# Performance work log

Measured on AMD Instinct MI355X. Metric: run time of the kernel, lower is better.

Reference implementation:

```python
import jax, jax.numpy as jnp
import numpy as np

N = 17
H = 8
DIRECT = np.array([[0,1],[1,2],[2,3],[0,4],[4,5],[5,6],[0,7],[7,8],[8,9],[9,10],[8,11],[11,12],[12,13],[8,14],[14,15],[15,16]])
SYM = np.array([[1,4],[2,5],[3,6],[11,14],[12,15],[13,16]])


def _base_mask(dw, sw, cw):
    # static skeleton bias: ones + direct-connect + symmetric + self-connect weights
    m = jnp.ones((N, N), jnp.float32)
    m = m.at[DIRECT[:, 0], DIRECT[:, 1]].add(dw)
    m = m.at[SYM[:, 0], SYM[:, 1]].add(sw)
    m = m.at[SYM[:, 1], SYM[:, 0]].add(sw)
    return m + cw * jnp.eye(N, dtype=jnp.float32)


def _ln_custom(x, g, b, eps=1e-6):
    # custom LayerNorm: unbiased std (torch .std default), eps added to std
    mu = x.mean(-1, keepdims=True)
    var = ((x - mu) ** 2).sum(-1, keepdims=True) / (x.shape[-1] - 1)
    return g * (x - mu) / (jnp.sqrt(var) + eps) + b


def _ln_std(x, g, b, eps=1e-5):
    # standard nn.LayerNorm (biased var, eps inside sqrt)
    mu = x.mean(-1, keepdims=True)
    var = ((x - mu) ** 2).mean(-1, keepdims=True)
    return g * (x - mu) * jax.lax.rsqrt(var + eps) + b


def _forward(mask, x, pre_3d, c, wq, bq, wk, bk, wv, bv, wo, bo, sa_w1, sa_b1, sa_g1, sa_sb1, sa_w2, sa_b2, sa_g2, sa_sb2, jrp_w, jrp_b, direct_w, sym_w, self_w, dyn_scale, A_hat, g1_w, g1_b, g2_w, g2_b, n1_g, n1_b, n2_g, n2_b, ada1_w, ada1_b, ada2_w, ada2_b):
    B, _, D = x.shape
    dk = D // H
    inv = 1.0 / np.sqrt(dk)
    mflag = (mask == 0)[:, None]                       # [B,1,N,N]
    sil_c = jax.nn.silu(c)
    for i in range(wq.shape[0]):                       # small fixed layer count
        # --- sublayer 0: adaLN-modulated skeleton-biased self-attention ---
        sh1, sc1, gt1 = jnp.split(sil_c @ ada1_w[i] + ada1_b[i], 3, axis=2)
        xin = _ln_custom(x, n1_g[i], n1_b[i]) * (1 + sc1) + sh1
        Q = (pre_3d @ wq[i] + bq[i]).reshape(B, N, H, dk).transpose(0, 2, 1, 3)
        K = (xin @ wk[i] + bk[i]).reshape(B, N, H, dk).transpose(0, 2, 1, 3)
        V = (xin @ wv[i] + bv[i]).reshape(B, N, H, dk).transpose(0, 2, 1, 3)
        scores = jnp.einsum('bhqd,bhkd->bhqk', Q, K) * inv
        # dynamic skeleton mask from query features (pre_3d)
        jf = jax.nn.relu(_ln_std(pre_3d @ sa_w1[i] + sa_b1[i], sa_g1[i], sa_sb1[i]))
        jf = jax.nn.relu(_ln_std(jf @ sa_w2[i] + sa_b2[i], sa_g2[i], sa_sb2[i]))
        dyn = jax.nn.sigmoid(jf @ jrp_w[i] + jrp_b[i]) * dyn_scale[i]   # [B,N,N]
        skel = _base_mask(direct_w[i], sym_w[i], self_w[i])[None] + dyn
        guided = jnp.where(mflag, -1e9, scores * skel[:, None])
        p = jax.nn.softmax(guided, axis=-1)
        att = jnp.einsum('bhqk,bhkd->bhqd', p, V).transpose(0, 2, 1, 3).reshape(B, N, D)
        x = x + gt1 * (att @ wo[i] + bo[i])
        # --- sublayer 1: adaLN-modulated GraphNet (2 Laplacian gconvs) ---
        sh2, sc2, gt2 = jnp.split(sil_c @ ada2_w[i] + ada2_b[i], 3, axis=2)
        y = _ln_custom(x, n2_g[i], n2_b[i]) * (1 + sc2) + sh2
        a = A_hat[i]
        dh = (a.sum(0) + 1e-5) ** -0.5                  # column-degree^{-1/2}
        Lm = dh[:, None] * a * dh[None, :]
        y0 = jax.nn.relu(jnp.einsum('ij,bjd->bid', Lm, y) @ g1_w[i] + g1_b[i])
        y1 = jnp.einsum('ij,bjd->bid', Lm, y0) @ g2_w[i] + g2_b[i]
        x = x + gt2 * y1
    return x


def setup_inputs():
    B, D, Lyr = 4096, 256, 2
    ki = iter(jax.random.split(jax.random.key(0), 32))
    rn = lambda *s: jax.random.normal(next(ki), s, jnp.float32) * 0.02
    z = lambda *s: jnp.zeros(s, jnp.float32)
    o = lambda *s: jnp.ones(s, jnp.float32)
    return {
        'x': jax.random.normal(next(ki), (B, N, D), jnp.float32),
        'pre_3d': jax.random.normal(next(ki), (B, N, D), jnp.float32),
        'c': jax.random.normal(next(ki), (B, N, D), jnp.float32),
        'mask': jnp.ones((B, N, N), jnp.int32),
        'wq': rn(Lyr, D, D), 'bq': z(Lyr, D),
        'wk': rn(Lyr, D, D), 'bk': z(Lyr, D),
        'wv': rn(Lyr, D, D), 'bv': z(Lyr, D),
        'wo': rn(Lyr, D, D), 'bo': z(Lyr, D),
        'sa_w1': rn(Lyr, D, D // 2), 'sa_b1': z(Lyr, D // 2),
        'sa_g1': o(Lyr, D // 2), 'sa_sb1': z(Lyr, D // 2),
        'sa_w2': rn(Lyr, D // 2, D // 4), 'sa_b2': z(Lyr, D // 4),
        'sa_g2': o(Lyr, D // 4), 'sa_sb2': z(Lyr, D // 4),
        'jrp_w': rn(Lyr, D // 4, N), 'jrp_b': z(Lyr, N),
        'direct_w': jnp.full((Lyr,), 2.0, jnp.float32),
        'sym_w': jnp.full((Lyr,), 1.5, jnp.float32),
        'self_w': jnp.full((Lyr,), 3.0, jnp.float32),
        'dyn_scale': jnp.full((Lyr,), 0.5, jnp.float32),
        'A_hat': jnp.tile(jnp.eye(N, dtype=jnp.float32)[None], (Lyr, 1, 1)),
        'g1_w': rn(Lyr, D, 2 * D), 'g1_b': z(Lyr, 2 * D),
        'g2_w': rn(Lyr, 2 * D, D), 'g2_b': z(Lyr, D),
        'n1_g': o(Lyr, D), 'n1_b': z(Lyr, D),
        'n2_g': o(Lyr, D), 'n2_b': z(Lyr, D),
        'ada1_w': rn(Lyr, D, 3 * D), 'ada1_b': z(Lyr, 3 * D),
        'ada2_w': rn(Lyr, D, 3 * D), 'ada2_b': z(Lyr, 3 * D),
    }


def reference(x, pre_3d, c, mask, wq, bq, wk, bk, wv, bv, wo, bo, sa_w1, sa_b1, sa_g1, sa_sb1, sa_w2, sa_b2, sa_g2, sa_sb2, jrp_w, jrp_b, direct_w, sym_w, self_w, dyn_scale, A_hat, g1_w, g1_b, g2_w, g2_b, n1_g, n1_b, n2_g, n2_b, ada1_w, ada1_b, ada2_w, ada2_b):
    return _forward(mask, x, pre_3d, c, wq, bq, wk, bk, wv, bv, wo, bo, sa_w1, sa_b1, sa_g1, sa_sb1, sa_w2, sa_b2, sa_g2, sa_sb2, jrp_w, jrp_b, direct_w, sym_w, self_w, dyn_scale, A_hat, g1_w, g1_b, g2_w, g2_b, n1_g, n1_b, n2_g, n2_b, ada1_w, ada1_b, ada2_w, ada2_b)
```

## Files before the change

### kernel.cpp

```cpp
#include <hip/hip_runtime.h>
#include <stdint.h>


#define BATCH 4096
#define NJ 17
#define NHEAD 8

typedef __bf16 bf16x8 __attribute__((ext_vector_type(8)));
typedef float f32x4 __attribute__((ext_vector_type(4)));

__device__ __forceinline__ float bf2f(unsigned short u){
  union { unsigned int i; float f; } v; v.i = ((unsigned int)u) << 16; return v.f;
}
__device__ __forceinline__ unsigned short f2bf(float f){
  union { float f; unsigned int i; } v; v.f = f;
  unsigned int i = v.i;
  return (unsigned short)((i + 0x7fffu + ((i >> 16) & 1u)) >> 16);
}
__device__ __forceinline__ float blo(unsigned int v){ union{unsigned int i;float f;}x; x.i=v<<16; return x.f; }
__device__ __forceinline__ float bhi(unsigned int v){ union{unsigned int i;float f;}x; x.i=v&0xffff0000u; return x.f; }

__device__ __forceinline__ void gload_lds16(const void* g, void* l) {
  __builtin_amdgcn_global_load_lds(
      (const __attribute__((address_space(1))) unsigned int*)g,
      (__attribute__((address_space(3))) unsigned int*)l, 16, 0, 0);
}

__global__ __launch_bounds__(256) void prep_kernel(
    const float* __restrict__ pre, const float* __restrict__ c,
    unsigned short* __restrict__ pre_bf, unsigned short* __restrict__ silc_bf)
{
  size_t i = (size_t)(blockIdx.x*256 + threadIdx.x)*4;
  float4 p = *(const float4*)(pre + i);
  float4 cv = *(const float4*)(c + i);
  float s0 = cv.x/(1.f+__expf(-cv.x));
  float s1 = cv.y/(1.f+__expf(-cv.y));
  float s2 = cv.z/(1.f+__expf(-cv.z));
  float s3 = cv.w/(1.f+__expf(-cv.w));
  uint2 po, so;
  po.x = (unsigned)f2bf(p.x) | ((unsigned)f2bf(p.y)<<16);
  po.y = (unsigned)f2bf(p.z) | ((unsigned)f2bf(p.w)<<16);
  so.x = (unsigned)f2bf(s0) | ((unsigned)f2bf(s1)<<16);
  so.y = (unsigned)f2bf(s2) | ((unsigned)f2bf(s3)<<16);
  *(uint2*)(pre_bf + i) = po;
  *(uint2*)(silc_bf + i) = so;
}

struct TJob { const float* src; unsigned short* dst; int K; int N; };
struct TJobs { TJob j[22]; };

__global__ __launch_bounds__(256) void transpose_kernel(TJobs jobs)
{
  TJob jb = jobs.j[blockIdx.y];
  int total = jb.K * jb.N;
  int idx = blockIdx.x*256 + threadIdx.x;
  if (idx >= total) return;
  int n = idx / jb.K;
  int k = idx - n*jb.K;
  jb.dst[idx] = f2bf(jb.src[(size_t)k*jb.N + n]);
}

__global__ void lm_kernel(const float* __restrict__ A_hat, float* __restrict__ LmOut)
{
  int L = blockIdx.x;
  const float* a = A_hat + L*289;
  float* Lm = LmOut + L*289;
  __shared__ float dh[17];
  int t = threadIdx.x;
  if (t < 17) {
    float s = 0;
    for (int i = 0; i < 17; i++) s += a[i*17 + t];
    dh[t] = 1.0f/sqrtf(s + 1e-5f);
  }
  __syncthreads();
  for (int i = t; i < 289; i += 64) {
    int qq = i/17, jj = i - qq*17;
    Lm[i] = dh[qq]*a[i]*dh[jj];
  }
}

__global__ __launch_bounds__(256) void lnmod_kernel(
    const float* __restrict__ x, const unsigned short* __restrict__ shsc,
    const float* __restrict__ g, const float* __restrict__ b,
    unsigned short* __restrict__ out)
{
  int row = blockIdx.x*4 + (threadIdx.x>>6);
  int lane = threadIdx.x & 63;
  const float4 v = *(const float4*)(x + (size_t)row*256 + lane*4);
  float s = v.x+v.y+v.z+v.w;
#pragma unroll
  for (int o=32;o;o>>=1) s += __shfl_down(s,o,64);
  float mu = __shfl(s,0,64) * (1.f/256.f);
  float d0=v.x-mu,d1=v.y-mu,d2=v.z-mu,d3=v.w-mu;
  float qq = d0*d0+d1*d1+d2*d2+d3*d3;
#pragma unroll
  for (int o=32;o;o>>=1) qq += __shfl_down(qq,o,64);
  qq = __shfl(qq,0,64);
  float rstd = 1.f/(sqrtf(qq*(1.f/255.f)) + 1e-6f);
  int c = lane*4;
  const float4 gv = *(const float4*)(g + c);
  const float4 bv = *(const float4*)(b + c);
  const uint2 shp = *(const uint2*)(shsc + (size_t)row*512 + c);
  const uint2 scp = *(const uint2*)(shsc + (size_t)row*512 + 256 + c);
  float o0 = (gv.x*d0*rstd + bv.x)*(1.f+blo(scp.x)) + blo(shp.x);
  float o1 = (gv.y*d1*rstd + bv.y)*(1.f+bhi(scp.x)) + bhi(shp.x);
  float o2 = (gv.z*d2*rstd + bv.z)*(1.f+blo(scp.y)) + blo(shp.y);
  float o3 = (gv.w*d3*rstd + bv.w)*(1.f+bhi(scp.y)) + bhi(shp.y);
  uint2 ov;
  ov.x = (unsigned)f2bf(o0) | ((unsigned)f2bf(o1)<<16);
  ov.y = (unsigned)f2bf(o2) | ((unsigned)f2bf(o3)<<16);
  *(uint2*)(out + (size_t)row*256 + c) = ov;
}

template<int C>
__global__ __launch_bounds__(256) void lnstd_relu_kernel(
    unsigned short* __restrict__ io, const float* __restrict__ g, const float* __restrict__ b)
{
  constexpr int EPL = C/64;
  int row = blockIdx.x*4 + (threadIdx.x>>6);
  int lane = threadIdx.x & 63;
  unsigned short* rp = io + (size_t)row*C + lane*EPL;
  float v[EPL];
  if constexpr (EPL == 2) { unsigned int u = *(const unsigned int*)rp; v[0]=blo(u); v[1]=bhi(u); }
  else { v[0] = bf2f(rp[0]); }
  float s = 0;
#pragma unroll
  for (int e=0;e<EPL;e++) s += v[e];
#pragma unroll
  for (int o=32;o;o>>=1) s += __shfl_down(s,o,64);
  float mu = __shfl(s,0,64) * (1.f/C);
  float qq = 0;
#pragma unroll
  for (int e=0;e<EPL;e++){ float d=v[e]-mu; qq += d*d; }
#pragma unroll
  for (int o=32;o;o>>=1) qq += __shfl_down(qq,o,64);
  qq = __shfl(qq,0,64);
  float rstd = rsqrtf(qq*(1.f/C) + 1e-5f);
  unsigned short ov[EPL];
#pragma unroll
  for (int e=0;e<EPL;e++){
    int ccol = lane*EPL + e;
    float o = fmaxf(g[ccol]*(v[e]-mu)*rstd + b[ccol], 0.f);
    ov[e] = f2bf(o);
  }
  if constexpr (EPL==2){ *(unsigned int*)rp = (unsigned)ov[0] | ((unsigned)ov[1]<<16); }
  else rp[0] = ov[0];
}

__global__ __launch_bounds__(256) void skel_kernel(
    const unsigned short* __restrict__ jf2, const unsigned short* __restrict__ jrpt,
    const float* __restrict__ jrp_b,
    const float* __restrict__ dwp, const float* __restrict__ swp,
    const float* __restrict__ cwp, const float* __restrict__ dsp,
    float* __restrict__ skel)
{
  int gid = blockIdx.x*256 + threadIdx.x;
  int row = gid / 17;
  int k = gid - row*17;
  int q = row % 17;
  const uint4* a = (const uint4*)(jf2 + (size_t)row*64);
  const uint4* w = (const uint4*)(jrpt + k*64);
  float acc = jrp_b[k];
#pragma unroll
  for (int c = 0; c < 8; c++) {
    uint4 ua = a[c], uw = w[c];
    acc += blo(ua.x)*blo(uw.x) + bhi(ua.x)*bhi(uw.x)
         + blo(ua.y)*blo(uw.y) + bhi(ua.y)*bhi(uw.y)
         + blo(ua.z)*blo(uw.z) + bhi(ua.z)*bhi(uw.z)
         + blo(ua.w)*blo(uw.w) + bhi(ua.w)*bhi(uw.w);
  }
  float sig = 1.f/(1.f + __expf(-acc));
  float base = 1.f;
  const int dqa[16] = {0,1,2,0,4,5,0,7,8,9,8,11,12,8,14,15};
  const int dka[16] = {1,2,3,4,5,6,7,8,9,10,11,12,13,14,15,16};
#pragma unroll
  for (int t = 0; t < 16; t++) if (q==dqa[t] && k==dka[t]) base += dwp[0];
  const int s0a[6] = {1,2,3,11,12,13};
  const int s1a[6] = {4,5,6,14,15,16};
#pragma unroll
  for (int t = 0; t < 6; t++) if ((q==s0a[t]&&k==s1a[t])||(q==s1a[t]&&k==s0a[t])) base += swp[0];
  if (q==k) base += cwp[0];
  skel[gid] = base + sig*dsp[0];
}

__device__ __forceinline__ void load16f(const unsigned short* p, float* f){
  const uint4* p4 = (const uint4*)p;
#pragma unroll
  for (int c=0;c<2;c++){
    uint4 u=p4[c];
    f[c*8+0]=blo(u.x); f[c*8+1]=bhi(u.x); f[c*8+2]=blo(u.y); f[c*8+3]=bhi(u.y);
    f[c*8+4]=blo(u.z); f[c*8+5]=bhi(u.z); f[c*8+6]=blo(u.w); f[c*8+7]=bhi(u.w);
  }
}

__global__ __launch_bounds__(320) void attn_kernel(
    const unsigned short* Q, const unsigned short* __restrict__ KV,
    const float* __restrict__ skel,
    const int* __restrict__ mask, unsigned short* att)
{
  __shared__ unsigned short kvs[17*512];
  __shared__ float sks[289];
  __shared__ int   mks[289];
  const int b = blockIdx.x;
  const int tid = threadIdx.x;

  const uint4* src = (const uint4*)(KV + (size_t)b*17*512);
  for (int i = tid; i < 1088; i += 320) ((uint4*)kvs)[i] = src[i];
  const float* skb = skel + (size_t)b*289;
  const int* mkb = mask + (size_t)b*289;
  for (int i = tid; i < 289; i += 320) { sks[i] = skb[i]; mks[i] = mkb[i]; }
  __syncthreads();
  if (tid >= 272) return;

  const int t2 = tid >> 1;
  const int dh = tid & 1;
  const int h = t2 / 17;
  const int q = t2 - h*17;
  const int col = h*32 + dh*16;
  size_t rq = ((size_t)(b*17+q))*256 + col;
  float qv[16];
  load16f(Q + rq, qv);

  float p[17];
  float mx = -3e38f;
#pragma unroll
  for (int k = 0; k < 17; k++) {
    const uint4* kp = (const uint4*)(kvs + k*512 + col);
    float s = 0;
#pragma unroll
    for (int c = 0; c < 2; c++) {
      uint4 u = kp[c];
      s += qv[c*8+0]*blo(u.x) + qv[c*8+1]*bhi(u.x)
         + qv[c*8+2]*blo(u.y) + qv[c*8+3]*bhi(u.y)
         + qv[c*8+4]*blo(u.z) + qv[c*8+5]*bhi(u.z)
         + qv[c*8+6]*blo(u.w) + qv[c*8+7]*bhi(u.w);
    }
    s += __shfl_xor(s, 1, 64);
    s *= 0.17677669529663687f;
    float gvl = (mks[q*17+k]==0) ? -1e9f : s*sks[q*17+k];
    p[k] = gvl;
    mx = fmaxf(mx, gvl);
  }
  float sum = 0;
#pragma unroll
  for (int k = 0; k < 17; k++){ p[k] = __expf(p[k]-mx); sum += p[k]; }
  float inv = 1.f/sum;
  float acc[16];
#pragma unroll
  for (int d=0; d<16; d++) acc[d]=0;
#pragma unroll
  for (int k = 0; k < 17; k++) {
    float pk = p[k]*inv;
    const uint4* vp = (const uint4*)(kvs + k*512 + 256 + col);
#pragma unroll
    for (int c=0;c<2;c++){
      uint4 u=vp[c];
      acc[c*8+0] += pk*blo(u.x); acc[c*8+1] += pk*bhi(u.x);
      acc[c*8+2] += pk*blo(u.y); acc[c*8+3] += pk*bhi(u.y);
      acc[c*8+4] += pk*blo(u.z); acc[c*8+5] += pk*bhi(u.z);
      acc[c*8+6] += pk*blo(u.w); acc[c*8+7] += pk*bhi(u.w);
    }
  }
  uint4 o[2];
#pragma unroll
  for (int c=0;c<2;c++){
    o[c].x = (unsigned)f2bf(acc[c*8+0]) | ((unsigned)f2bf(acc[c*8+1])<<16);
    o[c].y = (unsigned)f2bf(acc[c*8+2]) | ((unsigned)f2bf(acc[c*8+3])<<16);
    o[c].z = (unsigned)f2bf(acc[c*8+4]) | ((unsigned)f2bf(acc[c*8+5])<<16);
    o[c].w = (unsigned)f2bf(acc[c*8+6]) | ((unsigned)f2bf(acc[c*8+7])<<16);
  }
  uint4* op = (uint4*)(att + rq);
  op[0] = o[0]; op[1] = o[1];
}

template<int D>
__global__ __launch_bounds__(256) void lmapply_kernel(
    unsigned short* __restrict__ io, const float* __restrict__ Lm)
{
  __shared__ unsigned short ys[17*D];
  __shared__ float lms[289];
  int b = blockIdx.x;
  int tid = threadIdx.x;
  unsigned short* base = io + (size_t)b*17*D;
  constexpr int CH = 17*D/8;
  for (int i = tid; i < CH; i += 256) ((uint4*)ys)[i] = ((const uint4*)base)[i];
  for (int i = tid; i < 289; i += 256) lms[i] = Lm[i];
  __syncthreads();
#pragma unroll
  for (int c0 = 0; c0 < D; c0 += 256) {
    int c = c0 + tid;
    float yv[17];
#pragma unroll
    for (int j = 0; j < 17; j++) yv[j] = bf2f(ys[j*D + c]);
#pragma unroll
    for (int qi = 0; qi < 17; qi++) {
      float a = 0;
#pragma unroll
      for (int j = 0; j < 17; j++) a += lms[qi*17+j]*yv[j];
      base[qi*D + c] = f2bf(a);
    }
  }
}

template<int TM, int TN, int EPI>
__global__ __launch_bounds__(256) void gemm_kernel(
    const unsigned short* __restrict__ A, const unsigned short* __restrict__ Bt,
    const float* __restrict__ bias, unsigned short* __restrict__ outbf,
    float* __restrict__ x_io, const unsigned short* __restrict__ gt,
    int N, int K)
{
  int lane = threadIdx.x & 63;
  int wave = threadIdx.x >> 6;
  int lm = lane & 15, quad = lane >> 4;
  int wm0 = blockIdx.x*(2*TM*16) + (wave>>1)*(TM*16);
  int wn0 = blockIdx.y*(2*TN*16) + (wave&1)*(TN*16);
  const unsigned short* pa[TM];
  const unsigned short* pb[TN];
#pragma unroll
  for (int t=0;t<TM;t++) pa[t] = A + (size_t)(wm0 + t*16 + lm)*K + quad*8;
#pragma unroll
  for (int t=0;t<TN;t++) pb[t] = Bt + (size_t)(wn0 + t*16 + lm)*K + quad*8;
  f32x4 acc[TM][TN] = {};
  for (int kc = 0; kc < K; kc += 32) {
    bf16x8 af[TM], bfv[TN];
#pragma unroll
    for (int t=0;t<TM;t++) af[t] = *(const bf16x8*)(pa[t] + kc);
#pragma unroll
    for (int t=0;t<TN;t++) bfv[t] = *(const bf16x8*)(pb[t] + kc);
#pragma unroll
    for (int i=0;i<TM;i++)
#pragma unroll
      for (int j=0;j<TN;j++)
        acc[i][j] = __builtin_amdgcn_mfma_f32_16x16x32_bf16(af[i], bfv[j], acc[i][j], 0, 0, 0);
  }
#pragma unroll
  for (int j=0;j<TN;j++) {
    int col = wn0 + j*16 + lm;
    float bv = bias[col];
#pragma unroll
    for (int i=0;i<TM;i++) {
      int r0 = wm0 + i*16 + quad*4;
#pragma unroll
      for (int e=0;e<4;e++) {
        int rr = r0 + e;
        float v = acc[i][j][e] + bv;
        if (EPI == 0) {
          outbf[(size_t)rr*N + col] = f2bf(v);
        } else if (EPI == 1) {
          outbf[(size_t)rr*N + col] = f2bf(fmaxf(v, 0.f));
        } else {
          size_t xi = (size_t)rr*N + col;
          x_io[xi] += bf2f(gt[(size_t)rr*256 + col]) * v;
        }
      }
    }
  }
}

template<int EPI>
__global__ __launch_bounds__(256) void gemm_lds_kernel(
    const unsigned short* __restrict__ A, const unsigned short* __restrict__ Bt,
    const float* __restrict__ bias, const float* __restrict__ bias2,
    unsigned short* __restrict__ out1, int ld1,
    unsigned short* __restrict__ out2, int ld2, int splitN,
    float* __restrict__ x_io, const unsigned short* __restrict__ gt,
    int K)
{
  __shared__ unsigned short As[3][128*32];
  __shared__ unsigned short Bs[3][128*32];
  const int tid = threadIdx.x;
  const int lane = tid & 63;
  const int wave = tid >> 6;
  const int lm = lane & 15, quad = lane >> 4;

  const int gx = gridDim.x;
  const int nwg = gx * (int)gridDim.y;
  int flat = (int)blockIdx.y * gx + (int)blockIdx.x;
  int xcd = flat & 7, idx = flat >> 3;
  int qd = nwg >> 3, rm = nwg & 7;
  int wg = (xcd < rm ? xcd*(qd+1) : rm*(qd+1) + (xcd-rm)*qd) + idx;
  int by = wg / gx, bx = wg - by*gx;
  const int m0 = by * 128;
  const int n0 = bx * 128;
  const int wm = (wave >> 1) * 64;
  const int wn = (wave & 1) * 64;

  const int srow = tid >> 2;
  const int sslot = tid & 3;

  auto stage = [&](int buf, int kc) {
#pragma unroll
    for (int l = 0; l < 2; l++) {
      int rr = l*64 + srow;
      int gs = sslot ^ (rr & 3);
      gload_lds16(A + (size_t)(m0 + rr)*K + kc + gs*8, &As[buf][l*2048 + tid*8]);
      gload_lds16(Bt + (size_t)(n0 + rr)*K + kc + gs*8, &Bs[buf][l*2048 + tid*8]);
    }
  };

  const int nt = K >> 5;
  stage(0, 0);
  stage(1, 32);

  f32x4 acc[4][4] = {};
  for (int t = 0; t < nt; t++) {
    if (t + 2 < nt) {
      stage((t+2)%3, (t+2)*32);
      asm volatile("s_waitcnt vmcnt(8)" ::: "memory");
    } else if (t + 1 < nt) {
      asm volatile("s_waitcnt vmcnt(4)" ::: "memory");
    } else {
      asm volatile("s_waitcnt vmcnt(0)" ::: "memory");
    }
    __builtin_amdgcn_s_barrier();

    const unsigned short* as_ = As[t % 3];
    const unsigned short* bs_ = Bs[t % 3];
    bf16x8 af[4], bfv[4];
#pragma unroll
    for (int tt = 0; tt < 4; tt++) {
      int ra = wm + tt*16 + lm;
      af[tt]  = *(const bf16x8*)(as_ + ra*32 + ((quad ^ (ra & 3)) << 3));
      int rb = wn + tt*16 + lm;
      bfv[tt] = *(const bf16x8*)(bs_ + rb*32 + ((quad ^ (rb & 3)) << 3));
    }
#pragma unroll
    for (int i = 0; i < 4; i++)
#pragma unroll
      for (int j = 0; j < 4; j++)
        acc[i][j] = __builtin_amdgcn_mfma_f32_16x16x32_bf16(af[i], bfv[j], acc[i][j], 0, 0, 0);
    __builtin_amdgcn_s_barrier();
  }

#pragma unroll
  for (int j = 0; j < 4; j++) {
    int col = n0 + wn + j*16 + lm;
    float bv = (bias2 && col >= splitN) ? bias2[col - splitN] : bias[col];
#pragma unroll
    for (int i = 0; i < 4; i++) {
      int r0 = m0 + wm + i*16 + quad*4;
#pragma unroll
      for (int e = 0; e < 4; e++) {
        int rr = r0 + e;
        float v = acc[i][j][e] + bv;
        if (EPI == 0) {
          if (out2 && col >= splitN) out2[(size_t)rr*ld2 + (col - splitN)] = f2bf(v);
          else                       out1[(size_t)rr*ld1 + col] = f2bf(v);
        } else if (EPI == 1) {
          out1[(size_t)rr*ld1 + col] = f2bf(fmaxf(v, 0.f));
        } else {
          size_t xi = (size_t)rr*256 + col;
          x_io[xi] += bf2f(gt[xi]) * v;
        }
      }
    }
  }
}

extern "C" void kernel_launch(void* const* d_in, const int* in_sizes, int n_in,
                              void* d_out, int out_size, void* d_ws, size_t ws_size,
                              hipStream_t stream)
{
  const float* x_in = (const float*)d_in[0];
  const float* pre  = (const float*)d_in[1];
  const float* cc   = (const float*)d_in[2];
  const int*   mask = (const int*)d_in[3];
  const float* wq = (const float*)d_in[4];   const float* bq = (const float*)d_in[5];
  const float* wk = (const float*)d_in[6];   const float* bk = (const float*)d_in[7];
  const float* wv = (const float*)d_in[8];   const float* bvz = (const float*)d_in[9];
  const float* wo = (const float*)d_in[10];  const float* bo = (const float*)d_in[11];
  const float* sa_w1 = (const float*)d_in[12]; const float* sa_b1 = (const float*)d_in[13];
  const float* sa_g1 = (const float*)d_in[14]; const float* sa_sb1 = (const float*)d_in[15];
  const float* sa_w2 = (const float*)d_in[16]; const float* sa_b2 = (const float*)d_in[17];
  const float* sa_g2 = (const float*)d_in[18]; const float* sa_sb2 = (const float*)d_in[19];
  const float* jrp_w = (const float*)d_in[20]; const float* jrp_b = (const float*)d_in[21];
  const float* dwp = (const float*)d_in[22]; const float* swp = (const float*)d_in[23];
  const float* cwp = (const float*)d_in[24]; const float* dsp = (const float*)d_in[25];
  const float* A_hat = (const float*)d_in[26];
  const float* g1w = (const float*)d_in[27]; const float* g1b = (const float*)d_in[28];
  const float* g2w = (const float*)d_in[29]; const float* g2b = (const float*)d_in[30];
  const float* n1g = (const float*)d_in[31]; const float* n1b = (const float*)d_in[32];
  const float* n2g = (const float*)d_in[33]; const float* n2b = (const float*)d_in[34];
  const float* ada1w = (const float*)d_in[35]; const float* ada1b = (const float*)d_in[36];
  const float* ada2w = (const float*)d_in[37]; const float* ada2b = (const float*)d_in[38];

  char* ws = (char*)d_ws;
  size_t off = 0;
  auto alloc = [&](size_t bytes)->char* {
    char* p = ws + off; off = (off + bytes + 255) & ~(size_t)255; return p;
  };

  TJobs jobs;
  int ji = 0;
  auto addjob = [&](const float* src, unsigned short* dst, int Kd, int Nd) {
    jobs.j[ji].src = src; jobs.j[ji].dst = dst; jobs.j[ji].K = Kd; jobs.j[ji].N = Nd;
    ji++;
  };
  unsigned short *t_ada1[2], *t_qsa[2], *t_kv[2], *t_wo[2],
                 *t_sa2[2], *t_jrp[2], *t_g1[2], *t_g2[2], *t_ada2[2];
  for (int L = 0; L < 2; L++) {
    t_ada1[L] = (unsigned short*)alloc((size_t)768*256*2);
    addjob(ada1w + (size_t)L*256*768, t_ada1[L], 256, 768);
    t_qsa[L] = (unsigned short*)alloc((size_t)384*256*2);
    addjob(wq + (size_t)L*65536, t_qsa[L], 256, 256);
    addjob(sa_w1 + (size_t)L*256*128, t_qsa[L] + 256*256, 256, 128);
    t_kv[L] = (unsigned short*)alloc((size_t)512*256*2);
    addjob(wk + (size_t)L*65536, t_kv[L], 256, 256);
    addjob(wv + (size_t)L*65536, t_kv[L] + 256*256, 256, 256);
    t_wo[L] = (unsigned short*)alloc((size_t)256*256*2);
    addjob(wo + (size_t)L*65536, t_wo[L], 256, 256);
    t_sa2[L] = (unsigned short*)alloc((size_t)64*128*2);
    addjob(sa_w2 + (size_t)L*128*64, t_sa2[L], 128, 64);
    t_jrp[L] = (unsigned short*)alloc((size_t)17*64*2);
    addjob(jrp_w + (size_t)L*64*17, t_jrp[L], 64, 17);
    t_g1[L] = (unsigned short*)alloc((size_t)512*256*2);
    addjob(g1w + (size_t)L*256*512, t_g1[L], 256, 512);
    t_g2[L] = (unsigned short*)alloc((size_t)256*512*2);
    addjob(g2w + (size_t)L*512*256, t_g2[L], 512, 256);
    t_ada2[L] = (unsigned short*)alloc((size_t)768*256*2);
    addjob(ada2w + (size_t)L*256*768, t_ada2[L], 256, 768);
  }
  float* lmbuf = (float*)alloc(2*289*4);
  size_t fixed_bytes = off;

  int chunkB = BATCH;
  for (; chunkB > 256; chunkB >>= 1) {
    size_t R = (size_t)chunkB * NJ;
    if (fixed_bytes + R*3652 + 8*256 <= ws_size) break;
  }
  const size_t R = (size_t)chunkB * NJ;
  const int nchunks = BATCH / chunkB;

  unsigned short* pre_bf  = (unsigned short*)alloc(R*256*2);
  unsigned short* silc_bf = (unsigned short*)alloc(R*256*2);
  unsigned short* xinb    = (unsigned short*)alloc(R*256*2);
  unsigned short* qbuf    = (unsigned short*)alloc(R*256*2);
  unsigned short* gtbuf   = (unsigned short*)alloc(R*256*2);
  unsigned short* kvb     = (unsigned short*)alloc(R*512*2);
  float*          skelb   = (float*)alloc(R*NJ*4);

  unsigned short* jf1 = xinb;
  unsigned short* jf2 = xinb + R*128;

  float* xout = (float*)d_out;
  hipMemcpyAsync(xout, x_in, (size_t)BATCH*NJ*256*4, hipMemcpyDeviceToDevice, stream);
  transpose_kernel<<<dim3(768, 22), 256, 0, stream>>>(jobs);
  lm_kernel<<<2, 64, 0, stream>>>(A_hat, lmbuf);

  const int gX = (int)(R/128);
  const int g4 = (int)(R/4);

  for (int ch = 0; ch < nchunks; ch++) {
    const size_t r0 = (size_t)ch * R;
    const float* pre_c = pre + r0*256;
    const float* cc_c  = cc + r0*256;
    const int* mask_c  = mask + (size_t)ch*chunkB*289;
    float* x_c = xout + r0*256;

    prep_kernel<<<g4, 256, 0, stream>>>(pre_c, cc_c, pre_bf, silc_bf);

    for (int L = 0; L < 2; L++) {
      gemm_lds_kernel<0><<<dim3(6,gX),256,0,stream>>>(silc_bf, t_ada1[L],
          ada1b + L*768, nullptr, kvb, 512, gtbuf, 256, 512, nullptr, nullptr, 256);
      lnmod_kernel<<<g4,256,0,stream>>>(x_c, kvb, n1g + L*256, n1b + L*256, xinb);
      gemm_lds_kernel<0><<<dim3(4,gX),256,0,stream>>>(xinb, t_kv[L],
          bk + L*256, bvz + L*256, kvb, 512, nullptr, 0, 256, nullptr, nullptr, 256);
      gemm_lds_kernel<0><<<dim3(3,gX),256,0,stream>>>(pre_bf, t_qsa[L],
          bq + L*256, sa_b1 + L*128, qbuf, 256, jf1, 128, 256, nullptr, nullptr, 256);
      lnstd_relu_kernel<128><<<g4,256,0,stream>>>(jf1, sa_g1 + L*128, sa_sb1 + L*128);
      gemm_kernel<4,2,0><<<dim3(gX,1),256,0,stream>>>(jf1, t_sa2[L], sa_b2 + L*64, jf2, nullptr, nullptr, 64, 128);
      lnstd_relu_kernel<64><<<g4,256,0,stream>>>(jf2, sa_g2 + L*64, sa_sb2 + L*64);
      skel_kernel<<<(int)(R*NJ/256),256,0,stream>>>(jf2, t_jrp[L], jrp_b + L*17, dwp+L, swp+L, cwp+L, dsp+L, skelb);
      attn_kernel<<<chunkB,320,0,stream>>>(qbuf, kvb, skelb, mask_c, qbuf);
      gemm_lds_kernel<3><<<dim3(2,gX),256,0,stream>>>(qbuf, t_wo[L],
          bo + L*256, nullptr, nullptr, 0, nullptr, 0, 0, x_c, gtbuf, 256);
      gemm_lds_kernel<0><<<dim3(6,gX),256,0,stream>>>(silc_bf, t_ada2[L],
          ada2b + L*768, nullptr, kvb, 512, gtbuf, 256, 512, nullptr, nullptr, 256);
      lnmod_kernel<<<g4,256,0,stream>>>(x_c, kvb, n2g + L*256, n2b + L*256, xinb);
      lmapply_kernel<256><<<chunkB,256,0,stream>>>(xinb, lmbuf + L*289);
      gemm_lds_kernel<1><<<dim3(4,gX),256,0,stream>>>(xinb, t_g1[L],
          g1b + L*512, nullptr, kvb, 512, nullptr, 0, 0, nullptr, nullptr, 256);
      lmapply_kernel<512><<<chunkB,256,0,stream>>>(kvb, lmbuf + L*289);
      gemm_lds_kernel<3><<<dim3(2,gX),256,0,stream>>>(kvb, t_g2[L],
          g2b + L*256, nullptr, nullptr, 0, nullptr, 0, 0, x_c, gtbuf, 512);
    }
  }
}
```

Baseline: 1.602 ms.

## Load full 256-wide K chunk into LDS per stage instead of triple-buffered pipeline

Replaces the three-stage BK=32 software pipeline with a single large LDS tile covering 256 K-elements per load, using an 8-way XOR swizzle. This cuts the number of barriers and waitcnt stalls per block. In exchange, load and compute no longer overlap, and LDS use rises to 128KB, which limits occupancy to one block per CU.

```diff
diff --git a/kernel.cpp b/kernel.cpp
--- a/kernel.cpp
+++ b/kernel.cpp
@@ -366,8 +366,8 @@
     float* __restrict__ x_io, const unsigned short* __restrict__ gt,
     int K)
 {
-  __shared__ unsigned short As[3][128*32];
-  __shared__ unsigned short Bs[3][128*32];
+  __shared__ unsigned short As[128*256];
+  __shared__ unsigned short Bs[128*256];
   const int tid = threadIdx.x;
   const int lane = tid & 63;
   const int wave = tid >> 6;
@@ -385,51 +385,39 @@
   const int wm = (wave >> 1) * 64;
   const int wn = (wave & 1) * 64;
 
-  const int srow = tid >> 2;
-  const int sslot = tid & 3;
-
-  auto stage = [&](int buf, int kc) {
-#pragma unroll
-    for (int l = 0; l < 2; l++) {
-      int rr = l*64 + srow;
-      int gs = sslot ^ (rr & 3);
-      gload_lds16(A + (size_t)(m0 + rr)*K + kc + gs*8, &As[buf][l*2048 + tid*8]);
-      gload_lds16(Bt + (size_t)(n0 + rr)*K + kc + gs*8, &Bs[buf][l*2048 + tid*8]);
-    }
-  };
-
-  const int nt = K >> 5;
-  stage(0, 0);
-  stage(1, 32);
+  const int l5 = lane >> 5;
+  const int ls = lane & 31;
 
   f32x4 acc[4][4] = {};
-  for (int t = 0; t < nt; t++) {
-    if (t + 2 < nt) {
-      stage((t+2)%3, (t+2)*32);
-      asm volatile("s_waitcnt vmcnt(8)" ::: "memory");
-    } else if (t + 1 < nt) {
-      asm volatile("s_waitcnt vmcnt(4)" ::: "memory");
-    } else {
-      asm volatile("s_waitcnt vmcnt(0)" ::: "memory");
-    }
-    __builtin_amdgcn_s_barrier();
-
-    const unsigned short* as_ = As[t % 3];
-    const unsigned short* bs_ = Bs[t % 3];
-    bf16x8 af[4], bfv[4];
-#pragma unroll
-    for (int tt = 0; tt < 4; tt++) {
-      int ra = wm + tt*16 + lm;
-      af[tt]  = *(const bf16x8*)(as_ + ra*32 + ((quad ^ (ra & 3)) << 3));
-      int rb = wn + tt*16 + lm;
-      bfv[tt] = *(const bf16x8*)(bs_ + rb*32 + ((quad ^ (rb & 3)) << 3));
-    }
-#pragma unroll
-    for (int i = 0; i < 4; i++)
-#pragma unroll
-      for (int j = 0; j < 4; j++)
-        acc[i][j] = __builtin_amdgcn_mfma_f32_16x16x32_bf16(af[i], bfv[j], acc[i][j], 0, 0, 0);
-    __builtin_amdgcn_s_barrier();
+
+  for (int kc = 0; kc < K; kc += 256) {
+    if (kc) __syncthreads();
+#pragma unroll
+    for (int i = 0; i < 16; i++) {
+      int id2 = wave*16 + i;
+      int row = id2*2 + l5;
+      int slot = ls ^ (row & 7);
+      gload_lds16(A  + (size_t)(m0 + row)*K + kc + slot*8, As + id2*512 + lane*8);
+      gload_lds16(Bt + (size_t)(n0 + row)*K + kc + slot*8, Bs + id2*512 + lane*8);
+    }
+    __syncthreads();
+
+#pragma unroll
+    for (int k2 = 0; k2 < 8; k2++) {
+      bf16x8 af[4], bfv[4];
+#pragma unroll
+      for (int t = 0; t < 4; t++) {
+        int ra = wm + t*16 + lm;
+        af[t]  = *(const bf16x8*)(As + ra*256 + ((((k2<<2)|quad) ^ (ra & 7)) << 3));
+        int rb = wn + t*16 + lm;
+        bfv[t] = *(const bf16x8*)(Bs + rb*256 + ((((k2<<2)|quad) ^ (rb & 7)) << 3));
+      }
+#pragma unroll
+      for (int i = 0; i < 4; i++)
+#pragma unroll
+        for (int j = 0; j < 4; j++)
+          acc[i][j] = __builtin_amdgcn_mfma_f32_16x16x32_bf16(af[i], bfv[j], acc[i][j], 0, 0, 0);
+    }
   }
 
 #pragma unroll
```

Result: slower. 1.843 ms (+15.1%).

## Shrink LDS GEMM tiles to 64x64 with BK=64 double buffering

Applied to the files above, without the earlier changes.

Replaces the 128x128 output tile with a 32-wide K step and triple buffering in the LDS GEMM with a 64x64 tile, a 64-wide K step and double buffering. The swizzle widens to 8 slots and grids double in both dimensions. The aim is more workgroups and higher occupancy (launch bounds now request 4 blocks) for these narrow-N GEMMs over a moderately sized M. In exchange, each tile reuses operands less, so more global and LDS traffic per FLOP, and there is one fewer pipeline stage to hide load latency.

```diff
diff --git a/kernel.cpp b/kernel.cpp
--- a/kernel.cpp
+++ b/kernel.cpp
@@ -358,7 +358,7 @@
 }
 
 template<int EPI>
-__global__ __launch_bounds__(256) void gemm_lds_kernel(
+__global__ __launch_bounds__(256, 4) void gemm_lds_kernel(
     const unsigned short* __restrict__ A, const unsigned short* __restrict__ Bt,
     const float* __restrict__ bias, const float* __restrict__ bias2,
     unsigned short* __restrict__ out1, int ld1,
@@ -366,8 +366,8 @@
     float* __restrict__ x_io, const unsigned short* __restrict__ gt,
     int K)
 {
-  __shared__ unsigned short As[3][128*32];
-  __shared__ unsigned short Bs[3][128*32];
+  __shared__ unsigned short As[2][64*64];
+  __shared__ unsigned short Bs[2][64*64];
   const int tid = threadIdx.x;
   const int lane = tid & 63;
   const int wave = tid >> 6;
@@ -380,64 +380,64 @@
   int qd = nwg >> 3, rm = nwg & 7;
   int wg = (xcd < rm ? xcd*(qd+1) : rm*(qd+1) + (xcd-rm)*qd) + idx;
   int by = wg / gx, bx = wg - by*gx;
-  const int m0 = by * 128;
-  const int n0 = bx * 128;
-  const int wm = (wave >> 1) * 64;
-  const int wn = (wave & 1) * 64;
-
-  const int srow = tid >> 2;
-  const int sslot = tid & 3;
+  const int m0 = by * 64;
+  const int n0 = bx * 64;
+  const int wm = (wave >> 1) * 32;
+  const int wn = (wave & 1) * 32;
 
   auto stage = [&](int buf, int kc) {
 #pragma unroll
-    for (int l = 0; l < 2; l++) {
-      int rr = l*64 + srow;
-      int gs = sslot ^ (rr & 3);
-      gload_lds16(A + (size_t)(m0 + rr)*K + kc + gs*8, &As[buf][l*2048 + tid*8]);
-      gload_lds16(Bt + (size_t)(n0 + rr)*K + kc + gs*8, &Bs[buf][l*2048 + tid*8]);
+    for (int j = 0; j < 2; j++) {
+      int sidx = tid + 256*j;
+      int row = sidx >> 3;
+      int gs = (sidx & 7) ^ (row & 7);
+      gload_lds16(A  + (size_t)(m0 + row)*K + kc + gs*8, As[buf] + sidx*8);
+      gload_lds16(Bt + (size_t)(n0 + row)*K + kc + gs*8, Bs[buf] + sidx*8);
     }
   };
 
-  const int nt = K >> 5;
+  const int nt = K >> 6;
   stage(0, 0);
-  stage(1, 32);
-
-  f32x4 acc[4][4] = {};
+
+  f32x4 acc[2][2] = {};
+  int cur = 0;
   for (int t = 0; t < nt; t++) {
-    if (t + 2 < nt) {
-      stage((t+2)%3, (t+2)*32);
-      asm volatile("s_waitcnt vmcnt(8)" ::: "memory");
-    } else if (t + 1 < nt) {
+    if (t + 1 < nt) {
+      stage(cur ^ 1, (t+1)*64);
       asm volatile("s_waitcnt vmcnt(4)" ::: "memory");
     } else {
       asm volatile("s_waitcnt vmcnt(0)" ::: "memory");
     }
     __builtin_amdgcn_s_barrier();
 
-    const unsigned short* as_ = As[t % 3];
-    const unsigned short* bs_ = Bs[t % 3];
-    bf16x8 af[4], bfv[4];
-#pragma unroll
-    for (int tt = 0; tt < 4; tt++) {
-      int ra = wm + tt*16 + lm;
-      af[tt]  = *(const bf16x8*)(as_ + ra*32 + ((quad ^ (ra & 3)) << 3));
-      int rb = wn + tt*16 + lm;
-      bfv[tt] = *(const bf16x8*)(bs_ + rb*32 + ((quad ^ (rb & 3)) << 3));
-    }
-#pragma unroll
-    for (int i = 0; i < 4; i++)
-#pragma unroll
-      for (int j = 0; j < 4; j++)
-        acc[i][j] = __builtin_amdgcn_mfma_f32_16x16x32_bf16(af[i], bfv[j], acc[i][j], 0, 0, 0);
+    const unsigned short* as_ = As[cur];
+    const unsigned short* bs_ = Bs[cur];
+#pragma unroll
+    for (int kh = 0; kh < 2; kh++) {
+      bf16x8 af[2], bfv[2];
+#pragma unroll
+      for (int tt = 0; tt < 2; tt++) {
+        int ra = wm + tt*16 + lm;
+        af[tt]  = *(const bf16x8*)(as_ + ra*64 + ((((kh<<2)|quad) ^ (ra & 7)) << 3));
+        int rb = wn + tt*16 + lm;
+        bfv[tt] = *(const bf16x8*)(bs_ + rb*64 + ((((kh<<2)|quad) ^ (rb & 7)) << 3));
+      }
+#pragma unroll
+      for (int i = 0; i < 2; i++)
+#pragma unroll
+        for (int j = 0; j < 2; j++)
+          acc[i][j] = __builtin_amdgcn_mfma_f32_16x16x32_bf16(af[i], bfv[j], acc[i][j], 0, 0, 0);
+    }
     __builtin_amdgcn_s_barrier();
-  }
-
-#pragma unroll
-  for (int j = 0; j < 4; j++) {
+    cur ^= 1;
+  }
+
+#pragma unroll
+  for (int j = 0; j < 2; j++) {
     int col = n0 + wn + j*16 + lm;
     float bv = (bias2 && col >= splitN) ? bias2[col - splitN] : bias[col];
 #pragma unroll
-    for (int i = 0; i < 4; i++) {
+    for (int i = 0; i < 2; i++) {
       int r0 = m0 + wm + i*16 + quad*4;
 #pragma unroll
       for (int e = 0; e < 4; e++) {
@@ -548,6 +548,7 @@
   lm_kernel<<<2, 64, 0, stream>>>(A_hat, lmbuf);
 
   const int gX = (int)(R/128);
+  const int g64 = (int)(R/64);
   const int g4 = (int)(R/4);
 
   for (int ch = 0; ch < nchunks; ch++) {
@@ -560,28 +561,28 @@
     prep_kernel<<<g4, 256, 0, stream>>>(pre_c, cc_c, pre_bf, silc_bf);
 
     for (int L = 0; L < 2; L++) {
-      gemm_lds_kernel<0><<<dim3(6,gX),256,0,stream>>>(silc_bf, t_ada1[L],
+      gemm_lds_kernel<0><<<dim3(12,g64),256,0,stream>>>(silc_bf, t_ada1[L],
           ada1b + L*768, nullptr, kvb, 512, gtbuf, 256, 512, nullptr, nullptr, 256);
       lnmod_kernel<<<g4,256,0,stream>>>(x_c, kvb, n1g + L*256, n1b + L*256, xinb);
-      gemm_lds_kernel<0><<<dim3(4,gX),256,0,stream>>>(xinb, t_kv[L],
+      gemm_lds_kernel<0><<<dim3(8,g64),256,0,stream>>>(xinb, t_kv[L],
           bk + L*256, bvz + L*256, kvb, 512, nullptr, 0, 256, nullptr, nullptr, 256);
-      gemm_lds_kernel<0><<<dim3(3,gX),256,0,stream>>>(pre_bf, t_qsa[L],
+      gemm_lds_kernel<0><<<dim3(6,g64),256,0,stream>>>(pre_bf, t_qsa[L],
           bq + L*256, sa_b1 + L*128, qbuf, 256, jf1, 128, 256, nullptr, nullptr, 256);
       lnstd_relu_kernel<128><<<g4,256,0,stream>>>(jf1, sa_g1 + L*128, sa_sb1 + L*128);
       gemm_kernel<4,2,0><<<dim3(gX,1),256,0,stream>>>(jf1, t_sa2[L], sa_b2 + L*64, jf2, nullptr, nullptr, 64, 128);
       lnstd_relu_kernel<64><<<g4,256,0,stream>>>(jf2, sa_g2 + L*64, sa_sb2 + L*64);
       skel_kernel<<<(int)(R*NJ/256),256,0,stream>>>(jf2, t_jrp[L], jrp_b + L*17, dwp+L, swp+L, cwp+L, dsp+L, skelb);
       attn_kernel<<<chunkB,320,0,stream>>>(qbuf, kvb, skelb, mask_c, qbuf);
-      gemm_lds_kernel<3><<<dim3(2,gX),256,0,stream>>>(qbuf, t_wo[L],
+      gemm_lds_kernel<3><<<dim3(4,g64),256,0,stream>>>(qbuf, t_wo[L],
           bo + L*256, nullptr, nullptr, 0, nullptr, 0, 0, x_c, gtbuf, 256);
-      gemm_lds_kernel<0><<<dim3(6,gX),256,0,stream>>>(silc_bf, t_ada2[L],
+      gemm_lds_kernel<0><<<dim3(12,g64),256,0,stream>>>(silc_bf, t_ada2[L],
           ada2b + L*768, nullptr, kvb, 512, gtbuf, 256, 512, nullptr, nullptr, 256);
       lnmod_kernel<<<g4,256,0,stream>>>(x_c, kvb, n2g + L*256, n2b + L*256, xinb);
       lmapply_kernel<256><<<chunkB,256,0,stream>>>(xinb, lmbuf + L*289);
-      gemm_lds_kernel<1><<<dim3(4,gX),256,0,stream>>>(xinb, t_g1[L],
+      gemm_lds_kernel<1><<<dim3(8,g64),256,0,stream>>>(xinb, t_g1[L],
           g1b + L*512, nullptr, kvb, 512, nullptr, 0, 0, nullptr, nullptr, 256);
       lmapply_kernel<512><<<chunkB,256,0,stream>>>(kvb, lmbuf + L*289);
-      gemm_lds_kernel<3><<<dim3(2,gX),256,0,stream>>>(kvb, t_g2[L],
+      gemm_lds_kernel<3><<<dim3(4,g64),256,0,stream>>>(kvb, t_g2[L],
           g2b + L*256, nullptr, nullptr, 0, nullptr, 0, 0, x_c, gtbuf, 512);
     }
   }
```

After: 1.585 ms. About the same (-1.0%).
